# Optimization experiments

Measured on AMD Instinct MI355X. Metric: run time of the kernel, lower is better.

## Reference

```python
import jax, jax.numpy as jnp
import numpy as np

MIN_NORM = 1e-15
BALL_EPS = 0.004  # torch.float32 entry of BALL_EPS
SCALING = float(np.tanh(1.0 / 2.0))  # tanh(tau/2), tau=1.0
N_GRAPHS = 512
BN_EPS = 1e-5


def _cmin(v):
    return jnp.maximum(v, MIN_NORM)


def project(x):
    norm = _cmin(jnp.linalg.norm(x, axis=-1, keepdims=True))
    maxnorm = 1.0 - BALL_EPS
    return jnp.where(norm > maxnorm, x / norm * maxnorm, x)


def isometric_transform(x, a):
    r2 = jnp.sum(a * a, axis=-1, keepdims=True) - 1.0
    u = x - a
    return r2 / _cmin(jnp.sum(u * u, axis=-1, keepdims=True)) * u + a


def reflect_at_zero(x, mu):
    a = mu / _cmin(jnp.sum(mu * mu, axis=-1, keepdims=True))
    return isometric_transform(x, a)


def reflect_through_zero(p, q, x):
    p_ = p / _cmin(jnp.linalg.norm(p, axis=-1, keepdims=True))
    q_ = q / _cmin(jnp.linalg.norm(q, axis=-1, keepdims=True))
    r = q_ - p_
    m = jnp.sum(r * x, axis=-1, keepdims=True) / jnp.sum(r * r, axis=-1, keepdims=True)
    return x - 2.0 * r * m


def logmap0(y):
    yn = _cmin(jnp.linalg.norm(y, axis=-1, keepdims=True))
    return y / yn * jnp.arctanh(jnp.clip(yn, -1.0 + 1e-15, 1.0 - 1e-15))


def unique_rows(m):
    # Emulates torch.unique(dim=0, return_inverse=True) for all-distinct rows
    # (true w.p. 1 for continuous activations): lexicographic sort, col 0 primary.
    n = m.shape[0]
    perm = jnp.lexsort(m.T[::-1])
    inv = jnp.zeros(n, jnp.int32).at[perm].set(jnp.arange(n, dtype=jnp.int32))
    return m[perm], inv


def _forward(x, edge_index, batch, W0, b0, convW1, convb1, gamma, beta, convW2,
             convb2, fc1W, fc1b, fc2W, fc2b, fc3W, fc3b):
    n = x.shape[0]
    d = W0.shape[1]
    x = jax.nn.relu(x @ W0 + b0)
    xs = [x]
    z = [jnp.zeros((1, d), x.dtype)]
    inv = [jnp.zeros(n, jnp.int32)]
    u, iv = unique_rows(jax.lax.stop_gradient(x))  # no_grad in original
    z.append(SCALING * project(u))
    inv.append(iv)
    src, dst = edge_index[0], edge_index[1]
    n_layers = convW1.shape[0]
    p_vec = jnp.zeros((d,), x.dtype).at[-1].set(1.0)
    for i in range(n_layers):
        # GINConv (eps=0): MLP(x + sum_{j->i} x_j)
        agg = jax.ops.segment_sum(x[src], dst, num_segments=n)
        h = x + agg
        h = jax.nn.relu(h @ convW1[i] + convb1[i])
        mu = jnp.mean(h, axis=0)
        var = jnp.var(h, axis=0)  # biased, as BatchNorm1d training mode
        h = gamma[i] * (h - mu) / jnp.sqrt(var + BN_EPS) + beta[i]
        x = jax.nn.relu(h @ convW2[i] + convb2[i])
        x = x.at[:, -1].set(0.0)  # x @ diag zeroes last column
        xs.append(x)
        u_full, iv = unique_rows(jax.lax.stop_gradient(jnp.concatenate(xs, axis=1)))
        cnt = jax.ops.segment_sum(jnp.ones(n, jnp.int32), iv, num_segments=n)
        u = u_full[:, -d:]
        z_children = SCALING * project(u)
        t1 = jax.ops.segment_sum(inv[i + 1], iv, num_segments=n) // cnt
        z_current = z[i + 1][t1]
        t2 = jax.ops.segment_sum(inv[i], iv, num_segments=n) // cnt
        z_parent = z[i][t2]
        z_parent = reflect_at_zero(z_parent, z_current)
        z_children = reflect_through_zero(z_parent, p_vec, z_children)
        z_all = reflect_at_zero(z_children, z_current)
        inv.append(iv)
        z.append(z_all)
    xh = logmap0(z[-1])[inv[-1]]
    out = jax.ops.segment_sum(xh, batch, num_segments=N_GRAPHS)
    out = jax.nn.relu(out @ fc1W + fc1b)
    out = jax.nn.relu(out @ fc2W + fc2b)
    out = out @ fc3W + fc3b
    return jax.nn.log_softmax(out, axis=1)


def setup_inputs() -> dict:
    N, E, D_IN, D, L, C = 50000, 800000, 128, 64, 3, 10
    key = jax.random.key(0)
    ks = jax.random.split(key, 12)
    s = 0.05
    return {
        "x": jax.random.normal(ks[0], (N, D_IN), jnp.float32),
        "edge_index": jax.random.randint(ks[1], (2, E), 0, N),
        "batch": jnp.sort(jax.random.randint(ks[2], (N,), 0, 512)),
        "W0": jax.random.normal(ks[3], (D_IN, D), jnp.float32) * s,
        "b0": jnp.zeros((D,), jnp.float32),
        "convW1": jax.random.normal(ks[4], (L, D, D), jnp.float32) * s,
        "convb1": jnp.zeros((L, D), jnp.float32),
        "gamma": jnp.ones((L, D), jnp.float32),
        "beta": jnp.zeros((L, D), jnp.float32),
        "convW2": jax.random.normal(ks[5], (L, D, D), jnp.float32) * s,
        "convb2": jnp.zeros((L, D), jnp.float32),
        "fc1W": jax.random.normal(ks[6], (D, 128), jnp.float32) * s,
        "fc1b": jnp.zeros((128,), jnp.float32),
        "fc2W": jax.random.normal(ks[7], (128, 64), jnp.float32) * s,
        "fc2b": jnp.zeros((64,), jnp.float32),
        "fc3W": jax.random.normal(ks[8], (64, C), jnp.float32) * s,
        "fc3b": jnp.zeros((C,), jnp.float32),
    }


def reference(x, edge_index, batch, W0, b0, convW1, convb1, gamma, beta, convW2,
              convb2, fc1W, fc1b, fc2W, fc2b, fc3W, fc3b):
    return _forward(x, edge_index, batch, W0, b0, convW1, convb1, gamma, beta,
                    convW2, convb2, fc1W, fc1b, fc2W, fc2b, fc3W, fc3b)
```

## Files before the change

### kernel.cpp

```cpp
#include <hip/hip_runtime.h>
#include <hip/hip_fp16.h>
#include <math.h>

#define SCALING_F 0.46211715726000974f
#define MAXNORM_F 0.996f
#define MINNORM_F 1e-15f
#define BN_EPS_F  1e-5f

#define NBUCKET 32
#define CAP     64

typedef _Float16 v8h __attribute__((ext_vector_type(8)));
typedef float    v4f __attribute__((ext_vector_type(4)));

__device__ __forceinline__ float rsum16(float v) {
  v += __shfl_xor(v, 1, 64);
  v += __shfl_xor(v, 2, 64);
  v += __shfl_xor(v, 4, 64);
  v += __shfl_xor(v, 8, 64);
  return v;
}

__device__ __forceinline__ void rsum16x6(float& a, float& b, float& c,
                                         float& d, float& e, float& f) {
#pragma unroll
  for (int o = 1; o <= 8; o <<= 1) {
    a += __shfl_xor(a, o, 64);
    b += __shfl_xor(b, o, 64);
    c += __shfl_xor(c, o, 64);
    d += __shfl_xor(d, o, 64);
    e += __shfl_xor(e, o, 64);
    f += __shfl_xor(f, o, 64);
  }
}

__device__ __forceinline__ float h2f(float v) {
  return __half2float(__float2half(v));
}

__device__ __forceinline__ void acc8(float* a, uint4 u) {
  __half2 h0 = *(__half2*)&u.x;
  __half2 h1 = *(__half2*)&u.y;
  __half2 h2 = *(__half2*)&u.z;
  __half2 h3 = *(__half2*)&u.w;
  a[0] += __low2float(h0); a[1] += __high2float(h0);
  a[2] += __low2float(h1); a[3] += __high2float(h1);
  a[4] += __low2float(h2); a[5] += __high2float(h2);
  a[6] += __low2float(h3); a[7] += __high2float(h3);
}

__device__ __forceinline__ void load4f(const __half* p, float* a) {
  uint2 u = *(const uint2*)p;
  __half2 h0 = *(__half2*)&u.x;
  __half2 h1 = *(__half2*)&u.y;
  a[0] = __low2float(h0); a[1] = __high2float(h0);
  a[2] = __low2float(h1); a[3] = __high2float(h1);
}

__device__ __forceinline__ void zchain_row(
    int row, int i, bool valid,
    const __half* __restrict__ X0, const __half* __restrict__ X1,
    const __half* __restrict__ X2, const __half* __restrict__ X3,
    __half* __restrict__ Xh)
{
  float x0[4] = {0,0,0,0}, x1[4] = {0,0,0,0}, x2[4] = {0,0,0,0}, x3[4] = {0,0,0,0};
  if (valid) {
    load4f(&X0[(size_t)row * 64 + 4 * i], x0);
    load4f(&X1[(size_t)row * 64 + 4 * i], x1);
    load4f(&X2[(size_t)row * 64 + 4 * i], x2);
    load4f(&X3[(size_t)row * 64 + 4 * i], x3);
  }

  float zc[4], zp[4] = {0.f, 0.f, 0.f, 0.f};
  {
    float sx = rsum16(x0[0]*x0[0] + x0[1]*x0[1] + x0[2]*x0[2] + x0[3]*x0[3]);
    float norm = fmaxf(sqrtf(sx), MINNORM_F);
    float s = ((norm > MAXNORM_F) ? (MAXNORM_F / norm) : 1.0f) * SCALING_F;
#pragma unroll
    for (int e = 0; e < 4; ++e) zc[e] = x0[e] * s;
  }

  const float* Xi[3] = {x1, x2, x3};
#pragma unroll
  for (int li = 0; li < 3; ++li) {
    const float* xv = Xi[li];

    float p1 = xv[0]*xv[0] + xv[1]*xv[1] + xv[2]*xv[2] + xv[3]*xv[3];
    float p2 = zc[0]*zc[0]+zc[1]*zc[1]+zc[2]*zc[2]+zc[3]*zc[3];
    float p3 = zp[0]*zp[0]+zp[1]*zp[1]+zp[2]*zp[2]+zp[3]*zp[3];
    float p4 = zp[0]*zc[0]+zp[1]*zc[1]+zp[2]*zc[2]+zp[3]*zc[3];
    float p5 = zp[0]*xv[0]+zp[1]*xv[1]+zp[2]*xv[2]+zp[3]*xv[3];
    float p6 = zc[0]*xv[0]+zc[1]*xv[1]+zc[2]*xv[2]+zc[3]*xv[3];
    rsum16x6(p1, p2, p3, p4, p5, p6);
    float zc63 = __shfl(zc[3], 15, 16);
    float zp63 = __shfl(zp[3], 15, 16);

    float nzc2 = fmaxf(p2, MINNORM_F);
    float icz  = 1.0f / nzc2;
    float na2  = p2 * icz * icz;
    float r2   = na2 - 1.0f;
    float a63  = zc63 * icz;

    float sxn = fmaxf(sqrtf(p1), MINNORM_F);
    float sc  = ((sxn > MAXNORM_F) ? (MAXNORM_F / sxn) : 1.0f) * SCALING_F;
    float Sch2   = sc * sc * p1;
    float Szp_a  = p4 * icz;
    float Sa_ch  = sc * p6 * icz;
    float Szp_ch = sc * p5;
    float Su_a   = Szp_a - na2;
    float Su2    = p3 - 2.0f * Szp_a + na2;
    float nu2    = fmaxf(Su2, MINNORM_F);
    float t1     = r2 / nu2;
    float Szp22  = fmaxf(t1*t1*Su2 + 2.0f*t1*Su_a + na2, 0.0f);
    float npn    = fmaxf(sqrtf(Szp22), MINNORM_F);
    float ipn    = 1.0f / npn;
    float zp2_63 = t1 * (zp63 - a63) + a63;
    float Szp2ch = t1 * (Szp_ch - Sa_ch) + Sa_ch;
    float rdc    = -ipn * Szp2ch;
    float rdr    = 1.0f - 2.0f*ipn*zp2_63 + ipn*ipn*Szp22;
    float m2     = 2.0f * rdc / rdr;
    float Szp2a  = t1 * Su_a + na2;
    float Srr_a  = a63 - ipn * Szp2a;
    float Sc2a   = Sa_ch - m2 * Srr_a;
    float Sc22   = Sch2 - 2.0f*m2*rdc + m2*m2*rdr;
    float Sc2ma  = Sc22 - 2.0f*Sc2a + na2;
    float nu22   = fmaxf(Sc2ma, MINNORM_F);
    float t2     = r2 / nu22;

    float zn[4];
#pragma unroll
    for (int e = 0; e < 4; ++e) {
      float ai  = zc[e] * icz;
      float zp2 = t1 * (zp[e] - ai) + ai;
      float rri = ((i == 15 && e == 3) ? 1.0f : 0.0f) - ipn * zp2;
      float c2  = sc * xv[e] - m2 * rri;
      zn[e]     = t2 * (c2 - ai) + ai;
    }
#pragma unroll
    for (int e = 0; e < 4; ++e) { zp[e] = zc[e]; zc[e] = zn[e]; }
  }

  {
    float sz = rsum16(zc[0]*zc[0] + zc[1]*zc[1] + zc[2]*zc[2] + zc[3]*zc[3]);
    float yn  = fmaxf(sqrtf(sz), MINNORM_F);
    float t   = fminf(yn, 1.0f);
    float ath = 0.5f * logf((1.0f + t) / (1.0f - t));
    float wsc = ath / yn;
    if (valid) {
      __half hv[4];
      hv[0] = __float2half(zc[0] * wsc);
      hv[1] = __float2half(zc[1] * wsc);
      hv[2] = __float2half(zc[2] * wsc);
      hv[3] = __float2half(zc[3] * wsc);
      *(uint2*)&Xh[(size_t)row * 64 + 4 * i] = *(uint2*)hv;
    }
  }
}

__global__ __launch_bounds__(256) void k_zero(
    const float* __restrict__ W0, __half* __restrict__ W0T,
    int* __restrict__ zbase, int zwords)
{
  int id = blockIdx.x * 256 + threadIdx.x;
  if (id < 64 * 128) {
    int n = id >> 7, k = id & 127;
    W0T[id] = __float2half(W0[(size_t)k * 64 + n]);
  }
  const int stride = gridDim.x * 256;
  for (int z = id; z < zwords; z += stride) zbase[z] = 0;
}

__global__ __launch_bounds__(256) void k_front(
    const float* __restrict__ A, const __half* __restrict__ BT,
    const float* __restrict__ bias, __half* __restrict__ X, int M,
    const int* __restrict__ src, const int* __restrict__ dst, int E,
    int* __restrict__ cnt, unsigned short* __restrict__ slots,
    int* __restrict__ ovf,
    const int* __restrict__ batch, int G, int* __restrict__ gstart,
    const float* __restrict__ cW1, const float* __restrict__ cW2, int L,
    __half* __restrict__ W1T, __half* __restrict__ W2T,
    int DBLK, int MBLK, int GBLK)
{
  int bx = blockIdx.x;
  const int tid = threadIdx.x;

  if (bx < DBLK) {
    const int xcd   = bx & 7;
    const int chunk = bx >> 3;
    const int per   = (M + 7) >> 3;
    const int lo    = xcd * per;
    const int hi    = (lo + per < M) ? (lo + per) : M;
    int i0 = (chunk * 256 + tid) * 4;
    if (i0 + 4 <= E) {
      int4 d = *(const int4*)&dst[i0];
      int4 s = *(const int4*)&src[i0];
      if (d.x >= lo && d.x < hi) {
        int p = atomicAdd(&cnt[d.x], 1);
        if (p < CAP) slots[(size_t)d.x * CAP + p] = (unsigned short)s.x; else *ovf = 1;
      }
      if (d.y >= lo && d.y < hi) {
        int p = atomicAdd(&cnt[d.y], 1);
        if (p < CAP) slots[(size_t)d.y * CAP + p] = (unsigned short)s.y; else *ovf = 1;
      }
      if (d.z >= lo && d.z < hi) {
        int p = atomicAdd(&cnt[d.z], 1);
        if (p < CAP) slots[(size_t)d.z * CAP + p] = (unsigned short)s.z; else *ovf = 1;
      }
      if (d.w >= lo && d.w < hi) {
        int p = atomicAdd(&cnt[d.w], 1);
        if (p < CAP) slots[(size_t)d.w * CAP + p] = (unsigned short)s.w; else *ovf = 1;
      }
    } else {
      for (int i = i0; i < E; ++i) {
        int dv = dst[i];
        if (dv >= lo && dv < hi) {
          int p = atomicAdd(&cnt[dv], 1);
          if (p < CAP) slots[(size_t)dv * CAP + p] = (unsigned short)src[i];
          else *ovf = 1;
        }
      }
    }
    return;
  }
  bx -= DBLK;

  if (bx < MBLK) {
    const int w    = tid >> 6;
    const int lane = tid & 63;
    const int q    = lane >> 4;
    const int i    = lane & 15;
    const int rblk = bx * 64;
    const int arow = rblk + w * 16 + i;

    v4f acc[4];
#pragma unroll
    for (int t = 0; t < 4; ++t) acc[t] = (v4f){0.f, 0.f, 0.f, 0.f};

#pragma unroll
    for (int hh = 0; hh < 4; ++hh) {
      v8h af = (v8h){0, 0, 0, 0, 0, 0, 0, 0};
      if (arow < M) {
        const float* p = &A[(size_t)arow * 128 + hh * 32 + q * 8];
        float4 fa = *(const float4*)p;
        float4 fb = *(const float4*)(p + 4);
        af[0] = (_Float16)fa.x; af[1] = (_Float16)fa.y;
        af[2] = (_Float16)fa.z; af[3] = (_Float16)fa.w;
        af[4] = (_Float16)fb.x; af[5] = (_Float16)fb.y;
        af[6] = (_Float16)fb.z; af[7] = (_Float16)fb.w;
      }
#pragma unroll
      for (int t = 0; t < 4; ++t) {
        v8h bf = *(const v8h*)&BT[(size_t)(t * 16 + i) * 128 + hh * 32 + q * 8];
        acc[t] = __builtin_amdgcn_mfma_f32_16x16x32_f16(af, bf, acc[t], 0, 0, 0);
      }
    }

#pragma unroll
    for (int j = 0; j < 4; ++j) {
      int row = rblk + w * 16 + 4 * q + j;
      if (row >= M) continue;
#pragma unroll
      for (int t = 0; t < 4; ++t)
        X[(size_t)row * 64 + i + 16 * t] =
            __float2half(fmaxf(acc[t][j] + bias[i + 16 * t], 0.f));
    }
    return;
  }
  bx -= MBLK;

  if (bx < GBLK) {
    int r = bx * 256 + tid;
    if (r >= M) return;
    int b = batch[r];
    int prev = (r == 0) ? -1 : batch[r - 1];
    for (int g = prev + 1; g <= b; ++g) gstart[g] = r;
    if (r == M - 1)
      for (int g = b + 1; g <= G; ++g) gstart[g] = M;
    return;
  }
  bx -= GBLK;

  {
    int id = bx * 256 + tid;
    if (id < L * 64 * 64) {
      int l = id >> 12, rem = id & 4095;
      int n = rem >> 6, k = rem & 63;
      W1T[id] = __float2half(cW1[(size_t)l * 4096 + k * 64 + n]);
      W2T[id] = __float2half(cW2[(size_t)l * 4096 + k * 64 + n]);
    }
  }
}

__global__ __launch_bounds__(256) void k_pack3(
    const uint4* __restrict__ slotsIn, uint4* __restrict__ slotsOut, int nS,
    const uint4* __restrict__ x0In,    uint4* __restrict__ x0Out,    int nX,
    const uint4* __restrict__ cntIn,   uint4* __restrict__ cntOut,   int nC)
{
  int i = blockIdx.x * 256 + threadIdx.x;
  if (i < nS) { slotsOut[i] = slotsIn[i]; return; }
  i -= nS;
  if (i < nX) { x0Out[i] = x0In[i]; return; }
  i -= nX;
  if (i < nC) cntOut[i] = cntIn[i];
}

__global__ __launch_bounds__(256) void k_scan1(const int* __restrict__ ovf,
                                               const int* __restrict__ deg, int N,
                                               int* rowptr, int* bsum) {
  if (*ovf == 0) return;
  __shared__ int s[256];
  int t = threadIdx.x;
  int i = blockIdx.x * 256 + t;
  int v = (i < N) ? deg[i] : 0;
  s[t] = v;
  __syncthreads();
  for (int d = 1; d < 256; d <<= 1) {
    int add = (t >= d) ? s[t - d] : 0;
    __syncthreads();
    s[t] += add;
    __syncthreads();
  }
  if (i < N) rowptr[i] = s[t] - v;
  if (t == 255) bsum[blockIdx.x] = s[255];
}

__global__ __launch_bounds__(256) void k_scan2(const int* __restrict__ ovf,
                                               const int* __restrict__ bsum, int NB, int* boff) {
  if (*ovf == 0) return;
  __shared__ int s[256];
  int t = threadIdx.x;
  int v = (t < NB) ? bsum[t] : 0;
  s[t] = v;
  __syncthreads();
  for (int d = 1; d < 256; d <<= 1) {
    int add = (t >= d) ? s[t - d] : 0;
    __syncthreads();
    s[t] += add;
    __syncthreads();
  }
  boff[t] = s[t] - v;
}

__global__ __launch_bounds__(256) void k_scan3(const int* __restrict__ ovf,
                                               int* rowptr, const int* __restrict__ boff,
                                               int* cursor, int N, int E) {
  if (*ovf == 0) return;
  int i = blockIdx.x * 256 + threadIdx.x;
  if (i < N) {
    int v = rowptr[i] + boff[blockIdx.x];
    rowptr[i] = v;
    cursor[i] = v;
  }
  if (i == 0) rowptr[N] = E;
}

__global__ __launch_bounds__(256) void k_fill(const int* __restrict__ ovf,
                                              const int* __restrict__ src,
                                              const int* __restrict__ dst, int E,
                                              int* cursor, unsigned short* __restrict__ csr) {
  if (*ovf == 0) return;
  int i0 = (blockIdx.x * 256 + threadIdx.x) * 4;
  if (i0 + 4 <= E) {
    int4 d = *(const int4*)&dst[i0];
    int4 s = *(const int4*)&src[i0];
    int p0 = atomicAdd(&cursor[d.x], 1);
    int p1 = atomicAdd(&cursor[d.y], 1);
    int p2 = atomicAdd(&cursor[d.z], 1);
    int p3 = atomicAdd(&cursor[d.w], 1);
    csr[p0] = (unsigned short)s.x;
    csr[p1] = (unsigned short)s.y;
    csr[p2] = (unsigned short)s.z;
    csr[p3] = (unsigned short)s.w;
  } else {
    for (int i = i0; i < E; ++i) {
      int p = atomicAdd(&cursor[dst[i]], 1);
      csr[p] = (unsigned short)src[i];
    }
  }
}

__global__ __launch_bounds__(256, 4) void k_layer1(
    const __half* __restrict__ x,
    const int* __restrict__ ovf, const int* __restrict__ cnt,
    const unsigned short* __restrict__ slots,
    const int* __restrict__ rowptr, const unsigned short* __restrict__ csr,
    const __half* __restrict__ BT,
    const float* __restrict__ bias, __half* __restrict__ h,
    float* __restrict__ gstatP, int M)
{
  __shared__ __half AsH[16][80];
  const int tid  = threadIdx.x;
  const int w    = tid >> 6;
  const int lane = tid & 63;
  const int q    = lane >> 4;
  const int i    = lane & 15;
  const int g8   = lane >> 3;
  const int i8   = lane & 7;
  const int rblk = blockIdx.x * 16;

  const int r0 = rblk + w * 4 + 0;
  const int r1 = rblk + w * 4 + 1;
  const int r2 = rblk + w * 4 + 2;
  const int r3 = rblk + w * 4 + 3;
  const bool v0 = (r0 < M), v1 = (r1 < M), v2 = (r2 < M), v3 = (r3 < M);

  float a0[8] = {0.f,0.f,0.f,0.f,0.f,0.f,0.f,0.f};
  float a1[8] = {0.f,0.f,0.f,0.f,0.f,0.f,0.f,0.f};
  float a2[8] = {0.f,0.f,0.f,0.f,0.f,0.f,0.f,0.f};
  float a3[8] = {0.f,0.f,0.f,0.f,0.f,0.f,0.f,0.f};

  const unsigned short* idx;
  int c0 = 0, e0 = 0, c1 = 0, e1 = 0, c2 = 0, e2 = 0, c3 = 0, e3 = 0;
  if (*ovf == 0) {
    idx = slots;
    if (v0) { c0 = r0 * CAP; e0 = c0 + cnt[r0]; }
    if (v1) { c1 = r1 * CAP; e1 = c1 + cnt[r1]; }
    if (v2) { c2 = r2 * CAP; e2 = c2 + cnt[r2]; }
    if (v3) { c3 = r3 * CAP; e3 = c3 + cnt[r3]; }
  } else {
    idx = csr;
    if (v0) { c0 = rowptr[r0]; e0 = rowptr[r0 + 1]; }
    if (v1) { c1 = rowptr[r1]; e1 = rowptr[r1 + 1]; }
    if (v2) { c2 = rowptr[r2]; e2 = rowptr[r2 + 1]; }
    if (v3) { c3 = rowptr[r3]; e3 = rowptr[r3 + 1]; }
  }

  if (v0 && g8 == 0) acc8(a0, *(const uint4*)&x[(size_t)r0 * 64 + 8 * i8]);
  if (v1 && g8 == 0) acc8(a1, *(const uint4*)&x[(size_t)r1 * 64 + 8 * i8]);
  if (v2 && g8 == 0) acc8(a2, *(const uint4*)&x[(size_t)r2 * 64 + 8 * i8]);
  if (v3 && g8 == 0) acc8(a3, *(const uint4*)&x[(size_t)r3 * 64 + 8 * i8]);

  while ((c0 + 32 <= e0) | (c1 + 32 <= e1) | (c2 + 32 <= e2) | (c3 + 32 <= e3)) {
    const bool d0 = (c0 + 32 <= e0);
    const bool d1 = (c1 + 32 <= e1);
    const bool d2 = (c2 + 32 <= e2);
    const bool d3 = (c3 + 32 <= e3);
    int n0a=0,n0b=0,n0c=0,n0d=0, n1a=0,n1b=0,n1c=0,n1d=0;
    int n2a=0,n2b=0,n2c=0,n2d=0, n3a=0,n3b=0,n3c=0,n3d=0;
    if (d0) { n0a=idx[c0+g8]; n0b=idx[c0+8+g8]; n0c=idx[c0+16+g8]; n0d=idx[c0+24+g8]; }
    if (d1) { n1a=idx[c1+g8]; n1b=idx[c1+8+g8]; n1c=idx[c1+16+g8]; n1d=idx[c1+24+g8]; }
    if (d2) { n2a=idx[c2+g8]; n2b=idx[c2+8+g8]; n2c=idx[c2+16+g8]; n2d=idx[c2+24+g8]; }
    if (d3) { n3a=idx[c3+g8]; n3b=idx[c3+8+g8]; n3c=idx[c3+16+g8]; n3d=idx[c3+24+g8]; }
    uint4 u0a,u0b,u0c,u0d, u1a,u1b,u1c,u1d, u2a,u2b,u2c,u2d, u3a,u3b,u3c,u3d;
    if (d0) { u0a=*(const uint4*)&x[(size_t)n0a*64+8*i8]; u0b=*(const uint4*)&x[(size_t)n0b*64+8*i8];
              u0c=*(const uint4*)&x[(size_t)n0c*64+8*i8]; u0d=*(const uint4*)&x[(size_t)n0d*64+8*i8]; }
    if (d1) { u1a=*(const uint4*)&x[(size_t)n1a*64+8*i8]; u1b=*(const uint4*)&x[(size_t)n1b*64+8*i8];
              u1c=*(const uint4*)&x[(size_t)n1c*64+8*i8]; u1d=*(const uint4*)&x[(size_t)n1d*64+8*i8]; }
    if (d2) { u2a=*(const uint4*)&x[(size_t)n2a*64+8*i8]; u2b=*(const uint4*)&x[(size_t)n2b*64+8*i8];
              u2c=*(const uint4*)&x[(size_t)n2c*64+8*i8]; u2d=*(const uint4*)&x[(size_t)n2d*64+8*i8]; }
    if (d3) { u3a=*(const uint4*)&x[(size_t)n3a*64+8*i8]; u3b=*(const uint4*)&x[(size_t)n3b*64+8*i8];
              u3c=*(const uint4*)&x[(size_t)n3c*64+8*i8]; u3d=*(const uint4*)&x[(size_t)n3d*64+8*i8]; }
    if (d0) { acc8(a0,u0a); acc8(a0,u0b); acc8(a0,u0c); acc8(a0,u0d); c0 += 32; }
    if (d1) { acc8(a1,u1a); acc8(a1,u1b); acc8(a1,u1c); acc8(a1,u1d); c1 += 32; }
    if (d2) { acc8(a2,u2a); acc8(a2,u2b); acc8(a2,u2c); acc8(a2,u2d); c2 += 32; }
    if (d3) { acc8(a3,u3a); acc8(a3,u3b); acc8(a3,u3c); acc8(a3,u3d); c3 += 32; }
  }
  {
    const bool d0 = (c0 + 16 <= e0);
    const bool d1 = (c1 + 16 <= e1);
    const bool d2 = (c2 + 16 <= e2);
    const bool d3 = (c3 + 16 <= e3);
    int n0a=0,n0b=0, n1a=0,n1b=0, n2a=0,n2b=0, n3a=0,n3b=0;
    if (d0) { n0a = idx[c0 + g8]; n0b = idx[c0 + 8 + g8]; }
    if (d1) { n1a = idx[c1 + g8]; n1b = idx[c1 + 8 + g8]; }
    if (d2) { n2a = idx[c2 + g8]; n2b = idx[c2 + 8 + g8]; }
    if (d3) { n3a = idx[c3 + g8]; n3b = idx[c3 + 8 + g8]; }
    uint4 u0a,u0b,u1a,u1b,u2a,u2b,u3a,u3b;
    if (d0) { u0a=*(const uint4*)&x[(size_t)n0a*64+8*i8]; u0b=*(const uint4*)&x[(size_t)n0b*64+8*i8]; }
    if (d1) { u1a=*(const uint4*)&x[(size_t)n1a*64+8*i8]; u1b=*(const uint4*)&x[(size_t)n1b*64+8*i8]; }
    if (d2) { u2a=*(const uint4*)&x[(size_t)n2a*64+8*i8]; u2b=*(const uint4*)&x[(size_t)n2b*64+8*i8]; }
    if (d3) { u3a=*(const uint4*)&x[(size_t)n3a*64+8*i8]; u3b=*(const uint4*)&x[(size_t)n3b*64+8*i8]; }
    if (d0) { acc8(a0,u0a); acc8(a0,u0b); c0 += 16; }
    if (d1) { acc8(a1,u1a); acc8(a1,u1b); c1 += 16; }
    if (d2) { acc8(a2,u2a); acc8(a2,u2b); c2 += 16; }
    if (d3) { acc8(a3,u3a); acc8(a3,u3b); c3 += 16; }
  }
  {
    const bool d0 = (c0 + 8 <= e0);
    const bool d1 = (c1 + 8 <= e1);
    const bool d2 = (c2 + 8 <= e2);
    const bool d3 = (c3 + 8 <= e3);
    int n0 = 0, n1 = 0, n2 = 0, n3 = 0;
    if (d0) n0 = idx[c0 + g8];
    if (d1) n1 = idx[c1 + g8];
    if (d2) n2 = idx[c2 + g8];
    if (d3) n3 = idx[c3 + g8];
    uint4 u0, u1, u2, u3;
    if (d0) u0 = *(const uint4*)&x[(size_t)n0 * 64 + 8 * i8];
    if (d1) u1 = *(const uint4*)&x[(size_t)n1 * 64 + 8 * i8];
    if (d2) u2 = *(const uint4*)&x[(size_t)n2 * 64 + 8 * i8];
    if (d3) u3 = *(const uint4*)&x[(size_t)n3 * 64 + 8 * i8];
    if (d0) { acc8(a0, u0); c0 += 8; }
    if (d1) { acc8(a1, u1); c1 += 8; }
    if (d2) { acc8(a2, u2); c2 += 8; }
    if (d3) { acc8(a3, u3); c3 += 8; }
  }
  {
    const int rem0 = e0 - c0;
    const int rem1 = e1 - c1;
    const int rem2 = e2 - c2;
    const int rem3 = e3 - c3;
    int n0 = 0, n1 = 0, n2 = 0, n3 = 0;
    if (g8 < rem0) n0 = idx[c0 + g8];
    if (g8 < rem1) n1 = idx[c1 + g8];
    if (g8 < rem2) n2 = idx[c2 + g8];
    if (g8 < rem3) n3 = idx[c3 + g8];
    uint4 u0, u1, u2, u3;
    if (g8 < rem0) u0 = *(const uint4*)&x[(size_t)n0 * 64 + 8 * i8];
    if (g8 < rem1) u1 = *(const uint4*)&x[(size_t)n1 * 64 + 8 * i8];
    if (g8 < rem2) u2 = *(const uint4*)&x[(size_t)n2 * 64 + 8 * i8];
    if (g8 < rem3) u3 = *(const uint4*)&x[(size_t)n3 * 64 + 8 * i8];
    if (g8 < rem0) acc8(a0, u0);
    if (g8 < rem1) acc8(a1, u1);
    if (g8 < rem2) acc8(a2, u2);
    if (g8 < rem3) acc8(a3, u3);
  }

#pragma unroll
  for (int k = 0; k < 8; ++k) {
#pragma unroll
    for (int o = 8; o <= 32; o <<= 1) {
      a0[k] += __shfl_xor(a0[k], o, 64);
      a1[k] += __shfl_xor(a1[k], o, 64);
      a2[k] += __shfl_xor(a2[k], o, 64);
      a3[k] += __shfl_xor(a3[k], o, 64);
    }
  }
  if (g8 == 0) {
    __half hv[8];
#pragma unroll
    for (int k = 0; k < 8; ++k) hv[k] = __float2half(a0[k]);
    *(uint4*)&AsH[w * 4 + 0][8 * i8] = *(uint4*)hv;
#pragma unroll
    for (int k = 0; k < 8; ++k) hv[k] = __float2half(a1[k]);
    *(uint4*)&AsH[w * 4 + 1][8 * i8] = *(uint4*)hv;
#pragma unroll
    for (int k = 0; k < 8; ++k) hv[k] = __float2half(a2[k]);
    *(uint4*)&AsH[w * 4 + 2][8 * i8] = *(uint4*)hv;
#pragma unroll
    for (int k = 0; k < 8; ++k) hv[k] = __float2half(a3[k]);
    *(uint4*)&AsH[w * 4 + 3][8 * i8] = *(uint4*)hv;
  }
  __syncthreads();

  v4f acc = (v4f){0.f, 0.f, 0.f, 0.f};
#pragma unroll
  for (int hh = 0; hh < 2; ++hh) {
    v8h af = *(const v8h*)&AsH[i][hh * 32 + q * 8];
    v8h bf = *(const v8h*)&BT[(size_t)(w * 16 + i) * 64 + hh * 32 + q * 8];
    acc = __builtin_amdgcn_mfma_f32_16x16x32_f16(af, bf, acc, 0, 0, 0);
  }

  const int col = w * 16 + i;
  float s = 0.f, qq = 0.f;
#pragma unroll
  for (int j = 0; j < 4; ++j) {
    int row = rblk + 4 * q + j;
    if (row >= M) continue;
    float v = h2f(fmaxf(acc[j] + bias[col], 0.f));
    h[(size_t)row * 64 + col] = __float2half(v);
    s += v;
    qq += v * v;
  }
  s  += __shfl_xor(s, 16, 64);  qq += __shfl_xor(qq, 16, 64);
  s  += __shfl_xor(s, 32, 64);  qq += __shfl_xor(qq, 32, 64);
  if (q == 0) {
    const int bkt = (blockIdx.x & (NBUCKET - 1)) * 128;
    atomicAdd(&gstatP[bkt + col], s);
    atomicAdd(&gstatP[bkt + 64 + col], qq);
  }
}

__global__ __launch_bounds__(256) void k_layer2(
    const __half* __restrict__ A, const __half* __restrict__ BT,
    const float* __restrict__ bias,
    const float* __restrict__ gstat, const float* __restrict__ gamma,
    const float* __restrict__ beta,
    __half* __restrict__ Xout, int M,
    const __half* __restrict__ Z0, const __half* __restrict__ Z1,
    const __half* __restrict__ Z2, __half* __restrict__ Xh, int doZ)
{
  __shared__ float scl_s[64], shf_s[64];
  __shared__ float tmp[128];
  const int tid  = threadIdx.x;
  const int w    = tid >> 6;
  const int lane = tid & 63;
  const int q    = lane >> 4;
  const int i    = lane & 15;
  const int rblk = blockIdx.x * 64;
  const int arow = rblk + w * 16 + i;

  if (tid < 128) {
    float a = 0.f;
#pragma unroll
    for (int b2 = 0; b2 < NBUCKET; ++b2) a += gstat[b2 * 128 + tid];
    tmp[tid] = a;
  }
  __syncthreads();
  if (tid < 64) {
    float mu  = tmp[tid] / (float)M;
    float var = tmp[64 + tid] / (float)M - mu * mu;
    float sv  = gamma[tid] / sqrtf(var + BN_EPS_F);
    scl_s[tid] = sv;
    shf_s[tid] = beta[tid] - mu * sv;
  }
  __syncthreads();

  v4f acc[4];
#pragma unroll
  for (int t = 0; t < 4; ++t) acc[t] = (v4f){0.f, 0.f, 0.f, 0.f};
#pragma unroll
  for (int hh = 0; hh < 2; ++hh) {
    const int k0 = hh * 32 + q * 8;
    v8h af = (v8h){0, 0, 0, 0, 0, 0, 0, 0};
    {
      float hv[8] = {0,0,0,0,0,0,0,0};
      if (arow < M) {
        uint4 u = *(const uint4*)&A[(size_t)arow * 64 + k0];
        __half2 h0 = *(__half2*)&u.x;
        __half2 h1 = *(__half2*)&u.y;
        __half2 h2 = *(__half2*)&u.z;
        __half2 h3 = *(__half2*)&u.w;
        hv[0] = __low2float(h0); hv[1] = __high2float(h0);
        hv[2] = __low2float(h1); hv[3] = __high2float(h1);
        hv[4] = __low2float(h2); hv[5] = __high2float(h2);
        hv[6] = __low2float(h3); hv[7] = __high2float(h3);
      }
#pragma unroll
      for (int k = 0; k < 8; ++k)
        af[k] = (_Float16)fmaf(hv[k], scl_s[k0 + k], shf_s[k0 + k]);
    }
#pragma unroll
    for (int t = 0; t < 4; ++t) {
      v8h bf = *(const v8h*)&BT[(size_t)(t * 16 + i) * 64 + k0];
      acc[t] = __builtin_amdgcn_mfma_f32_16x16x32_f16(af, bf, acc[t], 0, 0, 0);
    }
  }

#pragma unroll
  for (int j = 0; j < 4; ++j) {
    int row = rblk + w * 16 + 4 * q + j;
    if (row >= M) continue;
#pragma unroll
    for (int t = 0; t < 4; ++t) {
      float v = fmaxf(acc[t][j] + bias[i + 16 * t], 0.f);
      if (i == 15 && t == 3) v = 0.f;
      Xout[(size_t)row * 64 + i + 16 * t] = __float2half(v);
    }
  }

  if (doZ) {
    __syncthreads();
    const int g16  = tid >> 4;
    const int il   = tid & 15;
#pragma unroll
    for (int p = 0; p < 4; ++p) {
      int row = rblk + p * 16 + g16;
      zchain_row(row, il, row < M, Z0, Z1, Z2, Xout, Xh);
    }
  }
}

__global__ __launch_bounds__(128) void k_mlp(const __half* __restrict__ Xh,
                                             const int* __restrict__ gstart,
                                             const float* __restrict__ fc1W, const float* __restrict__ fc1b,
                                             const float* __restrict__ fc2W, const float* __restrict__ fc2b,
                                             const float* __restrict__ fc3W, const float* __restrict__ fc3b,
                                             float* __restrict__ out) {
  __shared__ float p2s[2][64];
  __shared__ float p[64], o1[128], o2[64], lg[10], red[2];
  int g = blockIdx.x, t = threadIdx.x;
  int beg = gstart[g], end = gstart[g + 1];
  {
    int half = t >> 6, c = t & 63;
    float a = 0.f;
    int r = beg + half;
    for (; r + 6 <= end; r += 8) {
      float v0 = __half2float(Xh[(size_t)(r + 0) * 64 + c]);
      float v1 = __half2float(Xh[(size_t)(r + 2) * 64 + c]);
      float v2 = __half2float(Xh[(size_t)(r + 4) * 64 + c]);
      float v3 = __half2float(Xh[(size_t)(r + 6) * 64 + c]);
      a += (v0 + v1) + (v2 + v3);
    }
    for (; r < end; r += 2) a += __half2float(Xh[(size_t)r * 64 + c]);
    p2s[half][c] = a;
  }
  __syncthreads();
  if (t < 64) p[t] = p2s[0][t] + p2s[1][t];
  __syncthreads();
  {
    float a = fc1b[t];
    for (int k = 0; k < 64; ++k) a = fmaf(p[k], fc1W[k * 128 + t], a);
    o1[t] = fmaxf(a, 0.f);
  }
  __syncthreads();
  if (t < 64) {
    float a = fc2b[t];
    for (int k = 0; k < 128; ++k) a = fmaf(o1[k], fc2W[k * 64 + t], a);
    o2[t] = fmaxf(a, 0.f);
  }
  __syncthreads();
  if (t < 10) {
    float a = fc3b[t];
    for (int k = 0; k < 64; ++k) a = fmaf(o2[k], fc3W[k * 10 + t], a);
    lg[t] = a;
  }
  __syncthreads();
  if (t == 0) {
    float mx = lg[0];
    for (int j = 1; j < 10; ++j) mx = fmaxf(mx, lg[j]);
    float s = 0.f;
    for (int j = 0; j < 10; ++j) s += expf(lg[j] - mx);
    red[0] = mx;
    red[1] = logf(s);
  }
  __syncthreads();
  if (t < 10) out[(size_t)g * 10 + t] = lg[t] - red[0] - red[1];
}

extern "C" void kernel_launch(void* const* d_in, const int* in_sizes, int n_in,
                              void* d_out, int out_size, void* d_ws, size_t ws_size,
                              hipStream_t stream) {
  const float* x_in  = (const float*)d_in[0];
  const int*   ei    = (const int*)d_in[1];
  const int*   batch = (const int*)d_in[2];
  const float* W0    = (const float*)d_in[3];
  const float* b0    = (const float*)d_in[4];
  const float* cW1   = (const float*)d_in[5];
  const float* cb1   = (const float*)d_in[6];
  const float* gamma = (const float*)d_in[7];
  const float* beta  = (const float*)d_in[8];
  const float* cW2   = (const float*)d_in[9];
  const float* cb2   = (const float*)d_in[10];
  const float* fc1W  = (const float*)d_in[11];
  const float* fc1b  = (const float*)d_in[12];
  const float* fc2W  = (const float*)d_in[13];
  const float* fc2b  = (const float*)d_in[14];
  const float* fc3W  = (const float*)d_in[15];
  const float* fc3b  = (const float*)d_in[16];
  float* out = (float*)d_out;

  const int N = in_sizes[0] / 128;
  const int E = in_sizes[1] / 2;
  const int L = in_sizes[5] / (64 * 64);
  const int G = out_size / 10;
  const int* src = ei;
  const int* dst = ei + E;

  char* ws = (char*)d_ws;
  size_t off = 0;
  auto alloc = [&](size_t bytes) -> char* {
    char* p = ws + off;
    off += (bytes + 255) & ~(size_t)255;
    return p;
  };
  __half* X0  = (__half*)alloc((size_t)N * 64 * 2);
  __half* X0L = (__half*)alloc((size_t)N * 64 * 2);
  __half* X1  = (__half*)alloc((size_t)N * 64 * 2);
  __half* X2  = (__half*)alloc((size_t)N * 64 * 2);
  __half* X3  = (__half*)alloc((size_t)N * 64 * 2);
  __half* Bf  = (__half*)alloc((size_t)N * 64 * 2);
  __half* Xh  = (__half*)alloc((size_t)N * 64 * 2);
  __half* W0T = (__half*)alloc((size_t)64 * 128 * 2);
  __half* W1T = (__half*)alloc((size_t)L * 64 * 64 * 2);
  __half* W2T = (__half*)alloc((size_t)L * 64 * 64 * 2);
  int*    gstart = (int*)alloc((size_t)(G + 1) * 4);
  int*   cnt  = (int*)alloc((size_t)N * 4);
  float* gstatAll = (float*)alloc((size_t)3 * NBUCKET * 128 * 4);
  int*   ovf  = (int*)alloc(256);
  char*  zero_end = ws + off;
  int*   cnt2 = (int*)alloc((size_t)N * 4);
  unsigned short* slots  = (unsigned short*)alloc((size_t)N * CAP * 2);
  unsigned short* slots2 = (unsigned short*)alloc((size_t)N * CAP * 2);
  int*   rowptr = (int*)alloc((size_t)(N + 1) * 4);
  int*   cursor = (int*)alloc((size_t)N * 4);
  unsigned short* csr = (unsigned short*)alloc((size_t)E * 2);
  int*   bsum   = (int*)alloc(256 * 4);
  int*   boff   = (int*)alloc(256 * 4);
  __half* Xs[4] = {X0L, X1, X2, X3};

  const int zwords = (int)((zero_end - (char*)cnt) / 4);

  const int mmGrid    = (N + 63) / 64;
  const int l1Grid    = (N + 15) / 16;
  const int edge4Grid = (E / 4 + 255) / 256 + 1;
  const int fillGrid  = edge4Grid * 8;
  const int gbGrid    = (N + 255) / 256;
  const int wBlk      = (L * 4096 + 255) / 256;
  const int nS16      = N * CAP * 2 / 16;
  const int nX16      = N * 64 * 2 / 16;
  const int nC16      = (N * 4 + 15) / 16;
  const int packGrid  = (nS16 + nX16 + nC16 + 255) / 256;

  k_zero<<<256, 256, 0, stream>>>(W0, W0T, cnt, zwords);

  k_front<<<fillGrid + mmGrid + gbGrid + wBlk, 256, 0, stream>>>(
      x_in, W0T, b0, X0, N,
      src, dst, E, cnt, slots, ovf,
      batch, G, gstart,
      cW1, cW2, L, W1T, W2T,
      fillGrid, mmGrid, gbGrid);

  k_pack3<<<packGrid, 256, 0, stream>>>(
      (const uint4*)slots, (uint4*)slots2, nS16,
      (const uint4*)X0,    (uint4*)X0L,    nX16,
      (const uint4*)cnt,   (uint4*)cnt2,   nC16);

  const int NB = (N + 255) / 256;
  k_scan1<<<NB, 256, 0, stream>>>(ovf, cnt, N, rowptr, bsum);
  k_scan2<<<1, 256, 0, stream>>>(ovf, bsum, NB, boff);
  k_scan3<<<NB, 256, 0, stream>>>(ovf, rowptr, boff, cursor, N, E);
  k_fill<<<edge4Grid, 256, 0, stream>>>(ovf, src, dst, E, cursor, csr);

  for (int i = 0; i < L; ++i) {
    float* gstat = gstatAll + (size_t)i * NBUCKET * 128;
    const int doZ = (i == L - 1) ? 1 : 0;
    k_layer1<<<l1Grid, 256, 0, stream>>>(Xs[i], ovf, cnt2, slots2, rowptr, csr,
                                         W1T + (size_t)i * 4096, cb1 + i * 64,
                                         Bf, gstat, N);
    k_layer2<<<mmGrid, 256, 0, stream>>>(Bf, W2T + (size_t)i * 4096, cb2 + i * 64,
                                         gstat, gamma + i * 64, beta + i * 64,
                                         Xs[i + 1], N,
                                         Xs[0], X1, X2, Xh, doZ);
  }

  k_mlp<<<G, 128, 0, stream>>>(Xh, gstart, fc1W, fc1b, fc2W, fc2b, fc3W, fc3b, out);
}
```

Baseline: 339.4 us.

## Align layer1 row blocks with XCD-partitioned slot fill and drop slot copies

Stops copying the slots and count arrays into separate buffers. Instead, k_layer1 blocks are remapped so that each XCD (blockIdx & 7) handles the same contiguous row range that its k_front fill blocks wrote, which keeps the slot data local to that XCD's L2. The fill partition is changed to a multiple of 16 rows so the two mappings line up. This removes a large copy kernel's traffic, but it now depends on round-robin block-to-XCD dispatch for locality, and the grid may include some idle blocks past M.

```diff
diff --git a/kernel.cpp b/kernel.cpp
--- a/kernel.cpp
+++ b/kernel.cpp
@@ -179,7 +179,7 @@
     const int* __restrict__ batch, int G, int* __restrict__ gstart,
     const float* __restrict__ cW1, const float* __restrict__ cW2, int L,
     __half* __restrict__ W1T, __half* __restrict__ W2T,
-    int DBLK, int MBLK, int GBLK)
+    int per, int DBLK, int MBLK, int GBLK)
 {
   int bx = blockIdx.x;
   const int tid = threadIdx.x;
@@ -187,7 +187,6 @@
   if (bx < DBLK) {
     const int xcd   = bx & 7;
     const int chunk = bx >> 3;
-    const int per   = (M + 7) >> 3;
     const int lo    = xcd * per;
     const int hi    = (lo + per < M) ? (lo + per) : M;
     int i0 = (chunk * 256 + tid) * 4;
@@ -291,17 +290,11 @@
   }
 }
 
-__global__ __launch_bounds__(256) void k_pack3(
-    const uint4* __restrict__ slotsIn, uint4* __restrict__ slotsOut, int nS,
-    const uint4* __restrict__ x0In,    uint4* __restrict__ x0Out,    int nX,
-    const uint4* __restrict__ cntIn,   uint4* __restrict__ cntOut,   int nC)
+__global__ __launch_bounds__(256) void k_pack(
+    const uint4* __restrict__ in, uint4* __restrict__ out, int n16)
 {
   int i = blockIdx.x * 256 + threadIdx.x;
-  if (i < nS) { slotsOut[i] = slotsIn[i]; return; }
-  i -= nS;
-  if (i < nX) { x0Out[i] = x0In[i]; return; }
-  i -= nX;
-  if (i < nC) cntOut[i] = cntIn[i];
+  if (i < n16) out[i] = in[i];
 }
 
 __global__ __launch_bounds__(256) void k_scan1(const int* __restrict__ ovf,
@@ -386,7 +379,7 @@
     const int* __restrict__ rowptr, const unsigned short* __restrict__ csr,
     const __half* __restrict__ BT,
     const float* __restrict__ bias, __half* __restrict__ h,
-    float* __restrict__ gstatP, int M)
+    float* __restrict__ gstatP, int perBlk, int M)
 {
   __shared__ __half AsH[16][80];
   const int tid  = threadIdx.x;
@@ -396,7 +389,7 @@
   const int i    = lane & 15;
   const int g8   = lane >> 3;
   const int i8   = lane & 7;
-  const int rblk = blockIdx.x * 16;
+  const int rblk = (((blockIdx.x & 7) * perBlk) + (blockIdx.x >> 3)) * 16;
 
   const int r0 = rblk + w * 4 + 0;
   const int r1 = rblk + w * 4 + 1;
@@ -769,9 +762,7 @@
   float* gstatAll = (float*)alloc((size_t)3 * NBUCKET * 128 * 4);
   int*   ovf  = (int*)alloc(256);
   char*  zero_end = ws + off;
-  int*   cnt2 = (int*)alloc((size_t)N * 4);
-  unsigned short* slots  = (unsigned short*)alloc((size_t)N * CAP * 2);
-  unsigned short* slots2 = (unsigned short*)alloc((size_t)N * CAP * 2);
+  unsigned short* slots = (unsigned short*)alloc((size_t)N * CAP * 2);
   int*   rowptr = (int*)alloc((size_t)(N + 1) * 4);
   int*   cursor = (int*)alloc((size_t)N * 4);
   unsigned short* csr = (unsigned short*)alloc((size_t)E * 2);
@@ -781,16 +772,16 @@
 
   const int zwords = (int)((zero_end - (char*)cnt) / 4);
 
+  const int perBlk    = (N + 127) >> 7;
+  const int per       = perBlk * 16;
   const int mmGrid    = (N + 63) / 64;
-  const int l1Grid    = (N + 15) / 16;
+  const int l1Grid    = 8 * perBlk;
   const int edge4Grid = (E / 4 + 255) / 256 + 1;
   const int fillGrid  = edge4Grid * 8;
   const int gbGrid    = (N + 255) / 256;
   const int wBlk      = (L * 4096 + 255) / 256;
-  const int nS16      = N * CAP * 2 / 16;
   const int nX16      = N * 64 * 2 / 16;
-  const int nC16      = (N * 4 + 15) / 16;
-  const int packGrid  = (nS16 + nX16 + nC16 + 255) / 256;
+  const int packGrid  = (nX16 + 255) / 256;
 
   k_zero<<<256, 256, 0, stream>>>(W0, W0T, cnt, zwords);
 
@@ -799,12 +790,9 @@
       src, dst, E, cnt, slots, ovf,
       batch, G, gstart,
       cW1, cW2, L, W1T, W2T,
-      fillGrid, mmGrid, gbGrid);
-
-  k_pack3<<<packGrid, 256, 0, stream>>>(
-      (const uint4*)slots, (uint4*)slots2, nS16,
-      (const uint4*)X0,    (uint4*)X0L,    nX16,
-      (const uint4*)cnt,   (uint4*)cnt2,   nC16);
+      per, fillGrid, mmGrid, gbGrid);
+
+  k_pack<<<packGrid, 256, 0, stream>>>((const uint4*)X0, (uint4*)X0L, nX16);
 
   const int NB = (N + 255) / 256;
   k_scan1<<<NB, 256, 0, stream>>>(ovf, cnt, N, rowptr, bsum);
@@ -815,9 +803,9 @@
   for (int i = 0; i < L; ++i) {
     float* gstat = gstatAll + (size_t)i * NBUCKET * 128;
     const int doZ = (i == L - 1) ? 1 : 0;
-    k_layer1<<<l1Grid, 256, 0, stream>>>(Xs[i], ovf, cnt2, slots2, rowptr, csr,
+    k_layer1<<<l1Grid, 256, 0, stream>>>(Xs[i], ovf, cnt, slots, rowptr, csr,
                                          W1T + (size_t)i * 4096, cb1 + i * 64,
-                                         Bf, gstat, N);
+                                         Bf, gstat, perBlk, N);
     k_layer2<<<mmGrid, 256, 0, stream>>>(Bf, W2T + (size_t)i * 4096, cb2 + i * 64,
                                          gstat, gamma + i * 64, beta + i * 64,
                                          Xs[i + 1], N,
```

Measured after the change: 338.3 us. No clear change (-0.3%).
